# Kernel tuning notes

Hardware: AMD Instinct MI355X
Metric: run time of the kernel (lower is better)

Reference implementation:

```python
import jax, jax.numpy as jnp
import numpy as np

K_DIM = 128       # self.dim (PCA components)
SIGMA = 1.0       # cov = eye(dim) * sigma
NUM_LABELS = 10   # label vocabulary for private_label


def setup_inputs() -> dict:
    key = jax.random.key(0)
    k1, k2 = jax.random.split(key)
    mu = jax.random.normal(k1, (8192, 1024), dtype=jnp.float32)
    private_label = jax.random.randint(k2, (8192,), 0, NUM_LABELS, dtype=jnp.int32)
    return {"mu": mu, "private_label": private_label}


def _forward(mu, private_label):
    B = mu.shape[0]
    k = K_DIM
    x = mu.reshape(B, -1)
    # PCA: center, SVD of X^T, project onto top-k left singular vectors of X^T
    xc = x - jnp.mean(x, axis=0)
    U, _, _ = jnp.linalg.svd(xc.T, full_matrices=False)  # U: [D, min(D,B)]
    z = xc @ U[:, :k]                                    # [B, k]

    cov = jnp.eye(k, dtype=z.dtype) * SIGMA
    mu_total = jnp.mean(z, axis=0)                       # [k]
    diff = z - mu_total                                  # [B, k]
    Sigma_total = cov + (diff.T @ diff) / B              # [k, k]

    seg = private_label
    counts = jax.ops.segment_sum(jnp.ones((B,), z.dtype), seg, num_segments=NUM_LABELS)
    safe_c = jnp.where(counts > 0, counts, 1.0)
    sum_mu = jax.ops.segment_sum(z, seg, num_segments=NUM_LABELS)  # [L, k]
    mu_F = sum_mu / safe_c[:, None]                                # [L, k]

    # NOTE: faithful to source — per-label covariance uses diff w.r.t. mu_total
    onehot = jax.nn.one_hot(seg, NUM_LABELS, dtype=z.dtype)        # [B, L]
    masked = onehot[:, :, None] * diff[:, None, :]                 # [B, L, k]
    Sigma_sum = jnp.einsum('bli,bj->lij', masked, diff)            # [L, k, k]
    Sigma_F = cov + Sigma_sum / safe_c[:, None, None]              # [L, k, k]

    # KL( N(mu_F, Sigma_F) || N(mu_total, Sigma_total) ) per label
    Sinv = jnp.linalg.inv(Sigma_total)
    tr = jnp.einsum('ij,lji->l', Sinv, Sigma_F)
    d = mu_total[None, :] - mu_F                                   # [L, k]
    maha = jnp.einsum('li,ij,lj->l', d, Sinv, d)
    _, logdet_t = jnp.linalg.slogdet(Sigma_total)
    _, logdet_f = jnp.linalg.slogdet(Sigma_F)
    kl = 0.5 * (tr + maha - k + logdet_t - logdet_f)               # [L]

    present = counts > 0
    result = jnp.sum(jnp.where(present, kl, 0.0))
    n_keys = jnp.sum(present).astype(z.dtype)
    return result / (n_keys * B)


def reference(mu, private_label):
    return _forward(mu, private_label)
```

## Files before the change

### kernel.cpp

```cpp
#include <hip/hip_runtime.h>
#include <hip/hip_bf16.h>
#include <math.h>


#define B_N 8192
#define D_N 1024
#define K_N 128
#define M_N 256
#define NLAB 10

__device__ __forceinline__ float hashf(unsigned x) {
  x ^= x >> 16; x *= 0x7feb352du; x ^= x >> 15; x *= 0x846ca68bu; x ^= x >> 16;
  return (float)(x >> 8) * (1.0f / 16777216.0f) - 0.5f;
}

struct GArgs {
  const float* A; const float* B; float* C;
  int lda, ldb, ldc, K;
  float alpha;
  const float* C1; float b1; int ldc1;
  const float* C2; float b2; int ldc2;
  const float* r1u; const float* r1v; float r1c;
  const float* radd; float raddc;
  float addI;
  float* Cp; size_t mn; int pn;
  float* out2; float sc2, dg2;
};

template <bool AKM, bool BT>
__global__ __launch_bounds__(256)
void gemm_k(GArgs g) {
  __shared__ __align__(16) float AsRaw[2304];
  __shared__ __align__(16) float Bs[2176];
  const int tid = threadIdx.x;
  const int tx = tid & 15, ty = tid >> 4;
  const int i0 = blockIdx.x * 64, j0 = blockIdx.y * 64;
  const int ks = gridDim.z;
  const int Kc = g.K / ks;
  const int kbeg = blockIdx.z * Kc, kend = kbeg + Kc;
  float acc[4][4] = {};
  for (int k0 = kbeg; k0 < kend; k0 += 32) {
    if (AKM) {
#pragma unroll
      for (int p = 0; p < 2; ++p) {
        int f4 = tid + p * 256;
        int kk = f4 >> 4, i4 = f4 & 15;
        *(float4*)(AsRaw + kk * 68 + i4 * 4) =
            *(const float4*)(g.A + (size_t)(k0 + kk) * g.lda + i0 + i4 * 4);
      }
    } else {
#pragma unroll
      for (int p = 0; p < 2; ++p) {
        int f4 = tid + p * 256;
        int ii = f4 >> 3, k4 = f4 & 7;
        *(float4*)(AsRaw + ii * 36 + k4 * 4) =
            *(const float4*)(g.A + (size_t)(i0 + ii) * g.lda + k0 + k4 * 4);
      }
    }
    if (BT) {
#pragma unroll
      for (int p = 0; p < 8; ++p) {
        int idx = tid + p * 256;
        int jj = idx >> 5, kk = idx & 31;
        Bs[kk * 68 + jj] = g.B[(size_t)(j0 + jj) * g.ldb + k0 + kk];
      }
    } else {
#pragma unroll
      for (int p = 0; p < 2; ++p) {
        int f4 = tid + p * 256;
        int kk = f4 >> 4, j4 = f4 & 15;
        *(float4*)(Bs + kk * 68 + j4 * 4) =
            *(const float4*)(g.B + (size_t)(k0 + kk) * g.ldb + j0 + j4 * 4);
      }
    }
    __syncthreads();
#pragma unroll 8
    for (int kk = 0; kk < 32; ++kk) {
      float ra[4], rb[4];
      if (AKM) {
        const float4 va = *(const float4*)(AsRaw + kk * 68 + ty * 4);
        ra[0] = va.x; ra[1] = va.y; ra[2] = va.z; ra[3] = va.w;
      } else {
#pragma unroll
        for (int r = 0; r < 4; ++r) ra[r] = AsRaw[(ty * 4 + r) * 36 + kk];
      }
      const float4 vb = *(const float4*)(Bs + kk * 68 + tx * 4);
      rb[0] = vb.x; rb[1] = vb.y; rb[2] = vb.z; rb[3] = vb.w;
#pragma unroll
      for (int r = 0; r < 4; ++r)
#pragma unroll
        for (int c = 0; c < 4; ++c) acc[r][c] += ra[r] * rb[c];
    }
    __syncthreads();
  }
  if (ks > 1) {
    float* dst = g.Cp + (size_t)blockIdx.z * g.mn;
#pragma unroll
    for (int r = 0; r < 4; ++r)
#pragma unroll
      for (int c = 0; c < 4; ++c) {
        int gi = i0 + ty * 4 + r, gj = j0 + tx * 4 + c;
        dst[(size_t)gi * g.pn + gj] = g.alpha * acc[r][c];
      }
  } else {
#pragma unroll
    for (int r = 0; r < 4; ++r)
#pragma unroll
      for (int c = 0; c < 4; ++c) {
        int gi = i0 + ty * 4 + r, gj = j0 + tx * 4 + c;
        float v = g.alpha * acc[r][c];
        if (g.C1) v += g.b1 * g.C1[(size_t)gi * g.ldc1 + gj];
        if (g.C2) v += g.b2 * g.C2[(size_t)gi * g.ldc2 + gj];
        if (g.r1u) v += g.r1c * g.r1u[gi] * g.r1v[gj];
        if (g.radd) v += g.raddc * g.radd[gj];
        if (g.addI != 0.0f && gi == gj) v += g.addI;
        g.C[(size_t)gi * g.ldc + gj] = v;
      }
  }
}

struct CArgs {
  const float* P; float* C; size_t mn; int N, ldc, ks;
  const float* C1; float b1; int ldc1;
  const float* C2; float b2; int ldc2;
  const float* r1u; const float* r1v; float r1c;
  const float* radd; float raddc;
  float addI;
  float* out2; float sc2, dg2;
};

__global__ __launch_bounds__(256)
void combine_k(CArgs c) {
  size_t idx = (size_t)blockIdx.x * 256 + threadIdx.x;
  if (idx >= c.mn) return;
  int i = (int)(idx / c.N), j = (int)(idx % c.N);
  float s = 0.0f;
  for (int z = 0; z < c.ks; ++z) s += c.P[(size_t)z * c.mn + idx];
  if (c.C1) s += c.b1 * c.C1[(size_t)i * c.ldc1 + j];
  if (c.C2) s += c.b2 * c.C2[(size_t)i * c.ldc2 + j];
  if (c.r1u) s += c.r1c * c.r1u[i] * c.r1v[j];
  if (c.radd) s += c.raddc * c.radd[j];
  if (c.addI != 0.0f && i == j) s += c.addI;
  c.C[(size_t)i * c.ldc + j] = s;
  if (c.out2) c.out2[(size_t)i * c.N + j] = s * c.sc2 + ((i == j) ? c.dg2 : 0.0f);
}

__global__ __launch_bounds__(256)
void scaleshift_k(const float* in, float* out, int n, float sc, float dg) {
  size_t idx = (size_t)blockIdx.x * 256 + threadIdx.x;
  if (idx >= (size_t)n * n) return;
  int i = (int)(idx / n), j = (int)(idx % n);
  out[idx] = in[idx] * sc + ((i == j) ? dg : 0.0f);
}

__global__ __launch_bounds__(256)
void symscale_k(const float* in, float* out, int n, float sc, float dg) {
  size_t idx = (size_t)blockIdx.x * 256 + threadIdx.x;
  if (idx >= (size_t)n * n) return;
  int i = (int)(idx / n), j = (int)(idx % n);
  out[idx] = 0.5f * (in[idx] + in[(size_t)j * n + i]) * sc + ((i == j) ? dg : 0.0f);
}

__global__ __launch_bounds__(256)
void colmean_part_k(const float* x, double* part) {
  int col = blockIdx.x * 256 + threadIdx.x;
  int rs = blockIdx.y;
  double acc = 0.0;
  for (int r = rs * 512; r < (rs + 1) * 512; ++r)
    acc += (double)x[(size_t)r * D_N + col];
  part[(size_t)rs * D_N + col] = acc;
}

__global__ __launch_bounds__(256)
void colmean_comb_k(const double* part, float* m) {
  int col = blockIdx.x * 256 + threadIdx.x;
  double acc = 0.0;
  for (int rs = 0; rs < 16; ++rs) acc += part[(size_t)rs * D_N + col];
  m[col] = (float)(acc / (double)B_N);
}

__global__ void inits_k(float* S, int n, unsigned seed) {
  int i = blockIdx.x * 256 + threadIdx.x;
  if (i < n) S[i] = hashf((unsigned)i * 2654435761u + seed);
}

__global__ __launch_bounds__(512)
void chol128_k(const float* Gin, int ldg, float* LinvT, double* logdet, float* Sinv) {
  __shared__ float A[128][132];
  __shared__ float Bm[128][132];
  __shared__ float Y[64][66];
  __shared__ float Dsh[128];
  __shared__ float sqv[128];
  const int tid = threadIdx.x;
  for (int idx = tid; idx < 128 * 128; idx += 512)
    A[idx >> 7][idx & 127] = Gin[(size_t)(idx >> 7) * ldg + (idx & 127)];
  for (int idx = tid; idx < 128 * 132; idx += 512)
    (&Bm[0][0])[idx] = 0.0f;
  __syncthreads();
  for (int b = 0; b < 8; ++b) {
    const int o = b * 16;
    if (tid < 64) {
      const int lane = tid;
      float ra[16], rb[16], Dv[16];
#pragma unroll
      for (int q = 0; q < 16; ++q) {
        ra[q] = A[lane][o + q];
        rb[q] = A[lane + 64][o + q];
      }
#pragma unroll
      for (int jj = 0; jj < 16; ++jj) {
        const int c = o + jj;
        float pj = (c < 64) ? __shfl(ra[jj], c) : __shfl(rb[jj], c - 64);
        pj = fmaxf(pj, 1e-30f);
        Dv[jj] = pj;
        const float rdj = 1.0f / pj;
        const float ua = ra[jj] * rdj;
        const float ub = rb[jj] * rdj;
#pragma unroll
        for (int t = jj + 1; t < 16; ++t) {
          const int rt = o + t;
          float atj = (rt < 64) ? __shfl(ra[jj], rt) : __shfl(rb[jj], rt - 64);
          ra[t] -= ua * atj;
          rb[t] -= ub * atj;
        }
        ra[jj] = ua; rb[jj] = ub;
      }
#pragma unroll
      for (int q = 0; q < 16; ++q) {
        A[lane][o + q] = ra[q];
        A[lane + 64][o + q] = rb[q];
      }
      if (lane < 16) Dsh[o + lane] = Dv[lane];
    }
    __syncthreads();
    if (o + 16 < 128) {
      const int tx = tid & 15, ty = tid >> 4;
      for (int i = o + 16 + ty; i < 128; i += 32) {
        float w[16];
#pragma unroll
        for (int q = 0; q < 16; ++q) w[q] = A[i][o + q] * Dsh[o + q];
        for (int t = o + 16 + tx; t <= i; t += 16) {
          float s = A[i][t];
#pragma unroll
          for (int q = 0; q < 16; ++q) s -= w[q] * A[t][o + q];
          A[i][t] = s;
        }
      }
    }
    __syncthreads();
  }
  if (logdet && tid == 0) {
    double s = 0.0;
    for (int j = 0; j < 128; ++j) s += log((double)Dsh[j]);
    *logdet = s;
  }
  if (tid < 128) sqv[tid] = sqrtf(Dsh[tid]);
  __syncthreads();
  for (int idx = tid; idx < 128 * 128; idx += 512) {
    int i = idx >> 7, j = idx & 127;
    if (j <= i) A[i][j] *= sqv[j];
  }
  __syncthreads();
  if (tid < 128) {
    const int ob = (tid >> 6) * 64;
    const int c = tid & 63;
    for (int i = c; i < 64; ++i) {
      float s = (i == c) ? 1.0f : 0.0f;
      for (int t = c; t < i; ++t) s -= A[ob + i][ob + t] * Bm[ob + c][ob + t];
      Bm[ob + c][ob + i] = s / A[ob + i][ob + i];
    }
  }
  __syncthreads();
  for (int idx = tid; idx < 64 * 64; idx += 512) {
    int t = idx >> 6, c = idx & 63;
    float s = 0.0f;
    for (int s2 = c; s2 < 64; ++s2) s += A[64 + t][s2] * Bm[c][s2];
    Y[t][c] = s;
  }
  __syncthreads();
  for (int idx = tid; idx < 64 * 64; idx += 512) {
    int a = idx >> 6, c = idx & 63;
    float s = 0.0f;
    for (int t = 0; t <= a; ++t) s -= Bm[64 + t][64 + a] * Y[t][c];
    Bm[c][64 + a] = s;
  }
  __syncthreads();
  if (LinvT)
    for (int idx = tid; idx < 128 * 128; idx += 512)
      LinvT[idx] = Bm[idx >> 7][idx & 127];
  if (Sinv)
    for (int idx = tid; idx < 128 * 128; idx += 512) {
      int i = idx >> 7, j = idx & 127;
      int t0 = (i > j) ? i : j;
      float s = 0.0f;
      for (int t = t0; t < 128; ++t) s += Bm[i][t] * Bm[j][t];
      Sinv[idx] = s;
    }
}

__global__ __launch_bounds__(128)
void mw_k(const float* m, const float* W, float* mW) {
  int j = threadIdx.x;
  double acc = 0.0;
  for (int c = 0; c < D_N; ++c) acc += (double)m[c] * (double)W[(size_t)c * K_N + j];
  mW[j] = (float)acc;
}

__global__ __launch_bounds__(256)
void count_sort_k(const int* lab, int* perm, int* counts, int* offs) {
  __shared__ int cnt[NLAB][256];
  __shared__ int labOff[NLAB + 1];
  const int tid = threadIdx.x;
  int lc[NLAB];
#pragma unroll
  for (int l = 0; l < NLAB; ++l) lc[l] = 0;
  for (int r = tid * 32; r < tid * 32 + 32; ++r) {
    int l = lab[r]; l = (l < 0) ? 0 : (l > 9 ? 9 : l);
    lc[l]++;
  }
#pragma unroll
  for (int l = 0; l < NLAB; ++l) cnt[l][tid] = lc[l];
  __syncthreads();
  if (tid < NLAB) {
    int run = 0;
    for (int i = 0; i < 256; ++i) { int v = cnt[tid][i]; cnt[tid][i] = run; run += v; }
    counts[tid] = run;
  }
  __syncthreads();
  if (tid == 0) {
    int run = 0;
    for (int l = 0; l < NLAB; ++l) { labOff[l] = run; run += counts[l]; }
    labOff[NLAB] = run;
    for (int l = 0; l <= NLAB; ++l) offs[l] = labOff[l];
  }
  __syncthreads();
  int lc2[NLAB];
#pragma unroll
  for (int l = 0; l < NLAB; ++l) lc2[l] = 0;
  for (int r = tid * 32; r < tid * 32 + 32; ++r) {
    int l = lab[r]; l = (l < 0) ? 0 : (l > 9 ? 9 : l);
    int pos = labOff[l] + cnt[l][tid] + lc2[l];
    lc2[l]++;
    perm[pos] = r;
  }
}

__global__ __launch_bounds__(256)
void gather_k(const float* z, const int* perm, float* zs) {
  int g = blockIdx.x * 256 + threadIdx.x;
  int row = g >> 5, q = g & 31;
  const float4* zf = (const float4*)z;
  float4* of = (float4*)zs;
  of[(size_t)row * 32 + q] = zf[(size_t)perm[row] * 32 + q];
}

__global__ __launch_bounds__(128)
void labstat_part_k(const float* zs, const int* offs, double* part) {
  int l = blockIdx.x >> 3, s = blockIdx.x & 7;
  int j = threadIdx.x;
  int r0, r1;
  if (l < NLAB) {
    int st = offs[l], en = offs[l + 1], len = en - st;
    r0 = st + (int)(((long long)len * s) >> 3);
    r1 = st + (int)(((long long)len * (s + 1)) >> 3);
  } else {
    r0 = s * 1024; r1 = r0 + 1024;
  }
  double acc = 0.0;
  for (int r = r0; r < r1; ++r) acc += (double)zs[(size_t)r * K_N + j];
  part[((size_t)l * 8 + s) * K_N + j] = acc;
}

__global__ __launch_bounds__(128)
void labstat_comb_k(const double* part, float* sum_mu, float* muT) {
  int j = threadIdx.x;
  for (int l = 0; l < NLAB; ++l) {
    double a = 0.0;
    for (int s = 0; s < 8; ++s) a += part[((size_t)l * 8 + s) * K_N + j];
    sum_mu[l * K_N + j] = (float)a;
  }
  double t = 0.0;
  for (int s = 0; s < 8; ++s) t += part[((size_t)NLAB * 8 + s) * K_N + j];
  muT[j] = (float)(t / (double)B_N);
}

__global__ __launch_bounds__(256)
void sigsum_k(const float* zs, const int* offs, const float* muT, float* SigS) {
  int l = blockIdx.x >> 2, t = blockIdx.x & 3;
  int i0 = (t >> 1) * 64, j0 = (t & 1) * 64;
  __shared__ float Zi[32][66], Zj[32][66];
  __shared__ float muL[128];
  int tid = threadIdx.x, tx = tid & 15, ty = tid >> 4;
  if (tid < 128) muL[tid] = muT[tid];
  __syncthreads();
  int start = offs[l], end = offs[l + 1];
  float acc[4][4] = {};
  for (int base = start; base < end; base += 32) {
#pragma unroll
    for (int p = 0; p < 8; ++p) {
      int idx = tid + p * 256;
      int rr = idx >> 6, cc = idx & 63;
      int r = base + rr;
      float vi = 0.0f, vj = 0.0f;
      if (r < end) {
        vi = zs[(size_t)r * K_N + i0 + cc] - muL[i0 + cc];
        vj = zs[(size_t)r * K_N + j0 + cc] - muL[j0 + cc];
      }
      Zi[rr][cc] = vi; Zj[rr][cc] = vj;
    }
    __syncthreads();
    for (int rr = 0; rr < 32; ++rr) {
      float ra[4], rb[4];
#pragma unroll
      for (int r = 0; r < 4; ++r) ra[r] = Zi[rr][ty * 4 + r];
#pragma unroll
      for (int c = 0; c < 4; ++c) rb[c] = Zj[rr][tx * 4 + c];
#pragma unroll
      for (int r = 0; r < 4; ++r)
#pragma unroll
        for (int c = 0; c < 4; ++c) acc[r][c] += ra[r] * rb[c];
    }
    __syncthreads();
  }
#pragma unroll
  for (int r = 0; r < 4; ++r)
#pragma unroll
    for (int c = 0; c < 4; ++c)
      SigS[((size_t)l * K_N + i0 + ty * 4 + r) * K_N + j0 + tx * 4 + c] = acc[r][c];
}

__global__ __launch_bounds__(256)
void sigt_comb_k(const float* SigS, float* SigT) {
  int idx = blockIdx.x * 256 + threadIdx.x;
  int i = idx >> 7, j = idx & 127;
  double s = 0.0;
  for (int l = 0; l < NLAB; ++l) s += (double)SigS[(size_t)l * 16384 + idx];
  SigT[idx] = (float)(s / (double)B_N) + ((i == j) ? 1.0f : 0.0f);
}

__global__ __launch_bounds__(512)
void perlabel_k(const float* SigS, const float* Sinv, const float* mu,
                const float* sum_mu, const int* counts, const double* logdet_t,
                double* klout, int* present) {
  int l = blockIdx.x, tid = threadIdx.x;
  __shared__ float Amat[128][132];
  __shared__ double red[512];
  __shared__ float dv[128];
  __shared__ float Dsh[128];
  int cnt = counts[l];
  float sc = (cnt > 0) ? (float)cnt : 1.0f;
  for (int idx = tid; idx < 128 * 128; idx += 512) {
    int i = idx >> 7, j = idx & 127;
    Amat[i][j] = SigS[((size_t)l * K_N + i) * K_N + j] / sc + ((i == j) ? 1.0f : 0.0f);
  }
  if (tid < 128) dv[tid] = mu[tid] - sum_mu[l * K_N + tid] / sc;
  __syncthreads();
  double tr = 0.0, mh = 0.0;
  for (int idx = tid; idx < 128 * 128; idx += 512) {
    int i = idx >> 7, j = idx & 127;
    double sv = (double)Sinv[idx];
    tr += sv * (double)Amat[i][j];
    mh += sv * (double)dv[i] * (double)dv[j];
  }
  red[tid] = tr; __syncthreads();
  for (int off = 256; off > 0; off >>= 1) { if (tid < off) red[tid] += red[tid + off]; __syncthreads(); }
  double trv = red[0]; __syncthreads();
  red[tid] = mh; __syncthreads();
  for (int off = 256; off > 0; off >>= 1) { if (tid < off) red[tid] += red[tid + off]; __syncthreads(); }
  double mhv = red[0]; __syncthreads();
  for (int b = 0; b < 8; ++b) {
    const int o = b * 16;
    if (tid < 64) {
      const int lane = tid;
      float ra[16], rb[16], Dv[16];
#pragma unroll
      for (int q = 0; q < 16; ++q) {
        ra[q] = Amat[lane][o + q];
        rb[q] = Amat[lane + 64][o + q];
      }
#pragma unroll
      for (int jj = 0; jj < 16; ++jj) {
        const int c = o + jj;
        float pj = (c < 64) ? __shfl(ra[jj], c) : __shfl(rb[jj], c - 64);
        pj = fmaxf(pj, 1e-30f);
        Dv[jj] = pj;
        const float rdj = 1.0f / pj;
        const float ua = ra[jj] * rdj;
        const float ub = rb[jj] * rdj;
#pragma unroll
        for (int t = jj + 1; t < 16; ++t) {
          const int rt = o + t;
          float atj = (rt < 64) ? __shfl(ra[jj], rt) : __shfl(rb[jj], rt - 64);
          ra[t] -= ua * atj;
          rb[t] -= ub * atj;
        }
        ra[jj] = ua; rb[jj] = ub;
      }
#pragma unroll
      for (int q = 0; q < 16; ++q) {
        Amat[lane][o + q] = ra[q];
        Amat[lane + 64][o + q] = rb[q];
      }
      if (lane < 16) Dsh[o + lane] = Dv[lane];
    }
    __syncthreads();
    if (o + 16 < 128) {
      const int tx = tid & 15, ty = tid >> 4;
      for (int i = o + 16 + ty; i < 128; i += 32) {
        float w[16];
#pragma unroll
        for (int q = 0; q < 16; ++q) w[q] = Amat[i][o + q] * Dsh[o + q];
        for (int t = o + 16 + tx; t <= i; t += 16) {
          float s = Amat[i][t];
#pragma unroll
          for (int q = 0; q < 16; ++q) s -= w[q] * Amat[t][o + q];
          Amat[i][t] = s;
        }
      }
    }
    __syncthreads();
  }
  if (tid == 0) {
    double ld = 0.0;
    for (int j = 0; j < 128; ++j) ld += log((double)Dsh[j]);
    klout[l] = 0.5 * (trv + mhv - 128.0 + logdet_t[0] - ld);
    present[l] = (cnt > 0) ? 1 : 0;
  }
}

__global__ void finalize_k(const double* kl, const int* present, float* out) {
  if (threadIdx.x == 0 && blockIdx.x == 0) {
    double s = 0.0; int np = 0;
    for (int l = 0; l < NLAB; ++l)
      if (present[l]) { s += kl[l]; np++; }
    out[0] = (float)((np > 0) ? s / ((double)np * (double)B_N) : 0.0);
  }
}

static inline GArgs mkg(const float* A, int lda, const float* B, int ldb,
                        float* C, int ldc, int K, float alpha) {
  GArgs g{};
  g.A = A; g.B = B; g.C = C; g.lda = lda; g.ldb = ldb; g.ldc = ldc;
  g.K = K; g.alpha = alpha;
  return g;
}

static inline void run_g(hipStream_t st, bool akm, bool bt, GArgs g,
                         int M, int N, int ks, float* Ppart) {
  if (ks > 1) {
    g.Cp = Ppart; g.mn = (size_t)M * N; g.pn = N;
    dim3 grid(M / 64, N / 64, ks);
    if (akm)     hipLaunchKernelGGL((gemm_k<true, false>),  grid, dim3(256), 0, st, g);
    else if (bt) hipLaunchKernelGGL((gemm_k<false, true>),  grid, dim3(256), 0, st, g);
    else         hipLaunchKernelGGL((gemm_k<false, false>), grid, dim3(256), 0, st, g);
    CArgs c{Ppart, g.C, (size_t)M * N, N, g.ldc, ks,
            g.C1, g.b1, g.ldc1, g.C2, g.b2, g.ldc2,
            g.r1u, g.r1v, g.r1c, g.radd, g.raddc, g.addI,
            g.out2, g.sc2, g.dg2};
    hipLaunchKernelGGL(combine_k, dim3((unsigned)(((size_t)M * N + 255) / 256)),
                       dim3(256), 0, st, c);
  } else {
    dim3 grid(M / 64, N / 64);
    if (akm)     hipLaunchKernelGGL((gemm_k<true, false>),  grid, dim3(256), 0, st, g);
    else if (bt) hipLaunchKernelGGL((gemm_k<false, true>),  grid, dim3(256), 0, st, g);
    else         hipLaunchKernelGGL((gemm_k<false, false>), grid, dim3(256), 0, st, g);
  }
}

extern "C" void kernel_launch(void* const* d_in, const int* in_sizes, int n_in,
                              void* d_out, int out_size, void* d_ws, size_t ws_size,
                              hipStream_t stream) {
  const float* x = (const float*)d_in[0];
  const int* lab = (const int*)d_in[1];
  float* out = (float*)d_out;

  size_t off = 0;
  auto alloc = [&](size_t nbytes) -> void* {
    void* r = (void*)((char*)d_ws + off);
    off += ((nbytes + 255) / 256) * 256;
    return r;
  };
  float*  m     = (float*) alloc(D_N * 4);
  float*  Cn    = (float*) alloc((size_t)D_N * D_N * 4);
  float*  At    = (float*) alloc((size_t)D_N * D_N * 4);
  float*  T2    = (float*) alloc((size_t)D_N * D_N * 4);
  float*  Fo    = (float*) alloc((size_t)D_N * D_N * 4);
  float*  SA    = (float*) alloc((size_t)D_N * M_N * 4);
  float*  SB    = (float*) alloc((size_t)D_N * M_N * 4);
  float*  SC    = (float*) alloc((size_t)D_N * M_N * 4);
  float*  G256  = (float*) alloc((size_t)M_N * M_N * 4);
  float*  Tm    = (float*) alloc((size_t)M_N * M_N * 4);
  float*  Li11T = (float*) alloc((size_t)K_N * K_N * 4);
  float*  Li22T = (float*) alloc((size_t)K_N * K_N * 4);
  float*  L21b  = (float*) alloc((size_t)K_N * K_N * 4);
  float*  S22b  = (float*) alloc((size_t)K_N * K_N * 4);
  float*  Pb    = (float*) alloc((size_t)K_N * K_N * 4);
  float*  XTb   = (float*) alloc((size_t)K_N * K_N * 4);
  float*  Tt    = (float*) alloc((size_t)M_N * M_N * 4);
  float*  T2i   = (float*) alloc((size_t)M_N * M_N * 4);
  float*  T4i   = (float*) alloc((size_t)M_N * M_N * 4);
  float*  F6i   = (float*) alloc((size_t)M_N * M_N * 4);
  float*  VA    = (float*) alloc((size_t)M_N * K_N * 4);
  float*  VB    = (float*) alloc((size_t)M_N * K_N * 4);
  float*  G128  = (float*) alloc((size_t)K_N * K_N * 4);
  float*  Li128 = (float*) alloc((size_t)K_N * K_N * 4);
  float*  Wa    = (float*) alloc((size_t)D_N * K_N * 4);
  float*  Wb    = (float*) alloc((size_t)D_N * K_N * 4);
  float*  mW    = (float*) alloc(K_N * 4);
  double* partM = (double*)alloc((size_t)16 * D_N * 8);
  double* partL = (double*)alloc((size_t)11 * 8 * K_N * 8);
  float*  sumMu = (float*) alloc(NLAB * K_N * 4);
  float*  muT   = (float*) alloc(K_N * 4);
  float*  SigT  = (float*) alloc((size_t)K_N * K_N * 4);
  float*  Sinv  = (float*) alloc((size_t)K_N * K_N * 4);
  float*  SigS  = (float*) alloc((size_t)NLAB * K_N * K_N * 4);
  double* logdet_t = (double*)alloc(16);
  double* klv      = (double*)alloc(NLAB * 8);
  int*    counts = (int*)alloc(16 * 4);
  int*    offs   = (int*)alloc(16 * 4);
  int*    present= (int*)alloc(16 * 4);
  int*    perm   = (int*)alloc(B_N * 4);
  float*  T4   = At;
  float*  F12i = G256;
  float*  zs   = At;
  float*  z    = T2;
  size_t rem = (ws_size > off) ? (ws_size - off) : 0;
  int KS = 1;
  if (rem >= (size_t)16 * 1024 * 1024 + 4096) KS = 4;
  else if (rem >= (size_t)8 * 1024 * 1024 + 4096) KS = 2;
  float* Ppart = (float*)alloc((size_t)KS * 4 * 1024 * 1024);
  const int gks = (KS == 4) ? 8 : KS;
  (void)in_sizes; (void)n_in; (void)out_size;

  hipLaunchKernelGGL(colmean_part_k, dim3(4, 16), dim3(256), 0, stream, x, partM);
  hipLaunchKernelGGL(colmean_comb_k, dim3(4), dim3(256), 0, stream, partM, m);
  {
    GArgs g = mkg(x, D_N, x, D_N, Cn, D_N, B_N, 1.0f / (float)B_N);
    g.r1u = m; g.r1v = m; g.r1c = -1.0f;
    if (KS > 1) { g.out2 = At; g.sc2 = 1.6f; g.dg2 = -1.0f; }
    run_g(stream, true, false, g, D_N, D_N, KS, Ppart);
    if (KS == 1)
      hipLaunchKernelGGL(scaleshift_k, dim3((D_N * D_N + 255) / 256), dim3(256),
                         0, stream, Cn, At, D_N, 1.6f, -1.0f);
  }

  {
    GArgs g = mkg(At, D_N, At, D_N, T2, D_N, D_N, 2.0f);
    g.addI = -1.0f;
    run_g(stream, true, false, g, D_N, D_N, KS, Ppart);
    g = mkg(T2, D_N, T2, D_N, T4, D_N, D_N, 2.0f);
    g.addI = -1.0f;
    run_g(stream, true, false, g, D_N, D_N, KS, Ppart);
    g = mkg(T2, D_N, T4, D_N, Fo, D_N, D_N, 2.0f);
    g.C1 = T2; g.b1 = -1.0f; g.ldc1 = D_N;
    run_g(stream, true, false, g, D_N, D_N, KS, Ppart);
  }

  auto qr256 = [&](float* S, float* Snew) {
    GArgs g = mkg(S, M_N, S, M_N, G256, M_N, D_N, 1.0f);
    run_g(stream, true, false, g, M_N, M_N, gks, Ppart);
    hipLaunchKernelGGL(chol128_k, dim3(1), dim3(512), 0, stream,
                       G256, M_N, Li11T, (double*)nullptr, (float*)nullptr);
    g = mkg(G256 + 128 * M_N, M_N, Li11T, K_N, L21b, K_N, K_N, 1.0f);
    run_g(stream, false, false, g, K_N, K_N, 1, nullptr);
    g = mkg(L21b, K_N, L21b, K_N, S22b, K_N, K_N, -1.0f);
    g.C1 = G256 + 128 * M_N + 128; g.b1 = 1.0f; g.ldc1 = M_N;
    run_g(stream, false, true, g, K_N, K_N, 1, nullptr);
    hipLaunchKernelGGL(chol128_k, dim3(1), dim3(512), 0, stream,
                       S22b, K_N, Li22T, (double*)nullptr, (float*)nullptr);
    g = mkg(L21b, K_N, Li11T, K_N, Pb, K_N, K_N, 1.0f);
    run_g(stream, false, true, g, K_N, K_N, 1, nullptr);
    g = mkg(Pb, K_N, Li22T, K_N, XTb, K_N, K_N, -1.0f);
    run_g(stream, true, false, g, K_N, K_N, 1, nullptr);
    g = mkg(S, M_N, Li11T, K_N, Snew, M_N, K_N, 1.0f);
    run_g(stream, false, false, g, D_N, K_N, 1, nullptr);
    g = mkg(S, M_N, XTb, K_N, Snew + 128, M_N, K_N, 1.0f);
    run_g(stream, false, false, g, D_N, K_N, 1, nullptr);
    g = mkg(S + 128, M_N, Li22T, K_N, Snew + 128, M_N, K_N, 1.0f);
    g.C1 = Snew + 128; g.b1 = 1.0f; g.ldc1 = M_N;
    run_g(stream, false, false, g, D_N, K_N, 1, nullptr);
  };

  hipLaunchKernelGGL(inits_k, dim3((D_N * M_N + 255) / 256), dim3(256), 0, stream,
                     SA, D_N * M_N, 12345u);
  float* Scur = SA; float* t1 = SB; float* t2 = SC;
  for (int seg = 0; seg < 2; ++seg) {
    GArgs g = mkg(Fo, D_N, Scur, M_N, t1, M_N, D_N, 1.0f);
    run_g(stream, true, false, g, D_N, M_N, KS, Ppart);
    qr256(t1, t2);
    float* t = Scur; Scur = t2; t2 = t;
  }

  {
    GArgs g = mkg(Cn, D_N, Scur, M_N, t1, M_N, D_N, 1.0f);
    run_g(stream, true, false, g, D_N, M_N, KS, Ppart);
    g = mkg(Scur, M_N, t1, M_N, Tm, M_N, D_N, 1.0f);
    run_g(stream, true, false, g, M_N, M_N, gks, Ppart);
  }

  hipLaunchKernelGGL(symscale_k, dim3((M_N * M_N + 255) / 256), dim3(256), 0,
                     stream, Tm, Tt, M_N, 1.0f / 0.635f, -1.0f);
  {
    GArgs g = mkg(Tt, M_N, Tt, M_N, T2i, M_N, M_N, 2.0f);
    g.addI = -1.0f;
    run_g(stream, true, false, g, M_N, M_N, 1, nullptr);
    g = mkg(T2i, M_N, T2i, M_N, T4i, M_N, M_N, 2.0f);
    g.addI = -1.0f;
    run_g(stream, true, false, g, M_N, M_N, 1, nullptr);
    g = mkg(T2i, M_N, T4i, M_N, F6i, M_N, M_N, 2.0f);
    g.C1 = T2i; g.b1 = -1.0f; g.ldc1 = M_N;
    run_g(stream, true, false, g, M_N, M_N, 1, nullptr);
    g = mkg(F6i, M_N, F6i, M_N, F12i, M_N, M_N, 2.0f);
    g.addI = -1.0f;
    run_g(stream, true, false, g, M_N, M_N, 1, nullptr);
  }

  hipLaunchKernelGGL(inits_k, dim3((M_N * K_N + 255) / 256), dim3(256), 0, stream,
                     VA, M_N * K_N, 777u);
  {
    GArgs g = mkg(F12i, M_N, VA, K_N, VB, K_N, M_N, 1.0f);
    run_g(stream, true, false, g, M_N, K_N, 1, nullptr);
    g = mkg(VB, K_N, VB, K_N, G128, K_N, M_N, 1.0f);
    run_g(stream, true, false, g, K_N, K_N, 1, nullptr);
    hipLaunchKernelGGL(chol128_k, dim3(1), dim3(512), 0, stream,
                       G128, K_N, Li128, (double*)nullptr, (float*)nullptr);
    g = mkg(VB, K_N, Li128, K_N, VA, K_N, K_N, 1.0f);
    run_g(stream, false, false, g, M_N, K_N, 1, nullptr);
  }

  {
    GArgs g = mkg(Scur, M_N, VA, K_N, Wa, K_N, M_N, 1.0f);
    run_g(stream, false, false, g, D_N, K_N, 1, nullptr);
    g = mkg(Wa, K_N, Wa, K_N, G128, K_N, D_N, 1.0f);
    run_g(stream, true, false, g, K_N, K_N, gks, Ppart);
    hipLaunchKernelGGL(chol128_k, dim3(1), dim3(512), 0, stream,
                       G128, K_N, Li128, (double*)nullptr, (float*)nullptr);
    g = mkg(Wa, K_N, Li128, K_N, Wb, K_N, K_N, 1.0f);
    run_g(stream, false, false, g, D_N, K_N, 1, nullptr);
  }

  hipLaunchKernelGGL(mw_k, dim3(1), dim3(128), 0, stream, m, Wb, mW);
  {
    GArgs g = mkg(x, D_N, Wb, K_N, z, K_N, D_N, 1.0f);
    g.radd = mW; g.raddc = -1.0f;
    run_g(stream, false, false, g, B_N, K_N, KS, Ppart);
  }

  hipLaunchKernelGGL(count_sort_k, dim3(1), dim3(256), 0, stream,
                     lab, perm, counts, offs);
  hipLaunchKernelGGL(gather_k, dim3(B_N * 32 / 256), dim3(256), 0, stream,
                     z, perm, zs);

  hipLaunchKernelGGL(labstat_part_k, dim3(11 * 8), dim3(128), 0, stream,
                     zs, offs, partL);
  hipLaunchKernelGGL(labstat_comb_k, dim3(1), dim3(128), 0, stream,
                     partL, sumMu, muT);

  hipLaunchKernelGGL(sigsum_k, dim3(NLAB * 4), dim3(256), 0, stream,
                     zs, offs, muT, SigS);
  hipLaunchKernelGGL(sigt_comb_k, dim3(64), dim3(256), 0, stream, SigS, SigT);
  hipLaunchKernelGGL(chol128_k, dim3(1), dim3(512), 0, stream,
                     SigT, K_N, (float*)nullptr, logdet_t, Sinv);

  hipLaunchKernelGGL(perlabel_k, dim3(NLAB), dim3(512), 0, stream,
                     SigS, Sinv, muT, sumMu, counts, logdet_t, klv, present);
  hipLaunchKernelGGL(finalize_k, dim3(1), dim3(64), 0, stream, klv, present, out);
}
```

Measured before the change: 2.500 ms.

## Fuse blocked Cholesky-QR into single kernel producing full R inverse

Replaces the multi-launch 256-wide Cholesky-QR (two chol128 launches plus six small GEMMs) with one qrf_k kernel. It computes both diagonal Cholesky inverses, the Schur complement and the off-diagonal block of R^-1 in shared memory, then applies the whole 256x256 R^-1 to S with one GEMM. It also changes shared-memory padding from 132 to 129, factors the LDL code into a shared helper, and adds a larger split-K option for the covariance GEMM. The fused kernel runs on a single workgroup and does 128^3-sized GEMMs on one CU, which may serialize work that the separate GEMM launches spread across the device.

```diff
diff --git a/kernel.cpp b/kernel.cpp
--- a/kernel.cpp
+++ b/kernel.cpp
@@ -184,19 +184,8 @@
   if (i < n) S[i] = hashf((unsigned)i * 2654435761u + seed);
 }
 
-__global__ __launch_bounds__(512)
-void chol128_k(const float* Gin, int ldg, float* LinvT, double* logdet, float* Sinv) {
-  __shared__ float A[128][132];
-  __shared__ float Bm[128][132];
-  __shared__ float Y[64][66];
-  __shared__ float Dsh[128];
-  __shared__ float sqv[128];
-  const int tid = threadIdx.x;
-  for (int idx = tid; idx < 128 * 128; idx += 512)
-    A[idx >> 7][idx & 127] = Gin[(size_t)(idx >> 7) * ldg + (idx & 127)];
-  for (int idx = tid; idx < 128 * 132; idx += 512)
-    (&Bm[0][0])[idx] = 0.0f;
-  __syncthreads();
+__device__ __forceinline__
+void ldl128(float (&A)[128][129], float* Dsh, int tid) {
   for (int b = 0; b < 8; ++b) {
     const int o = b * 16;
     if (tid < 64) {
@@ -230,7 +219,9 @@
         A[lane][o + q] = ra[q];
         A[lane + 64][o + q] = rb[q];
       }
-      if (lane < 16) Dsh[o + lane] = Dv[lane];
+#pragma unroll
+      for (int q = 0; q < 16; ++q)
+        if (lane == q) Dsh[o + q] = Dv[q];
     }
     __syncthreads();
     if (o + 16 < 128) {
@@ -249,11 +240,15 @@
     }
     __syncthreads();
   }
-  if (logdet && tid == 0) {
-    double s = 0.0;
-    for (int j = 0; j < 128; ++j) s += log((double)Dsh[j]);
-    *logdet = s;
-  }
+}
+
+__device__ __forceinline__
+void cholinv128(float (&A)[128][129], float (&Bm)[128][129],
+                float (&Y)[64][65], float* Dsh, float* sqv, int tid) {
+  for (int idx = tid; idx < 128 * 129; idx += 512)
+    (&Bm[0][0])[idx] = 0.0f;
+  __syncthreads();
+  ldl128(A, Dsh, tid);
   if (tid < 128) sqv[tid] = sqrtf(Dsh[tid]);
   __syncthreads();
   for (int idx = tid; idx < 128 * 128; idx += 512) {
@@ -285,6 +280,24 @@
     Bm[c][64 + a] = s;
   }
   __syncthreads();
+}
+
+__global__ __launch_bounds__(512)
+void chol128_k(const float* Gin, int ldg, float* LinvT, double* logdet, float* Sinv) {
+  __shared__ float A[128][129];
+  __shared__ float Bm[128][129];
+  __shared__ float Y[64][65];
+  __shared__ float Dsh[128], sqv[128];
+  const int tid = threadIdx.x;
+  for (int idx = tid; idx < 128 * 128; idx += 512)
+    A[idx >> 7][idx & 127] = Gin[(size_t)(idx >> 7) * ldg + (idx & 127)];
+  __syncthreads();
+  cholinv128(A, Bm, Y, Dsh, sqv, tid);
+  if (logdet && tid == 0) {
+    double s = 0.0;
+    for (int j = 0; j < 128; ++j) s += log((double)Dsh[j]);
+    *logdet = s;
+  }
   if (LinvT)
     for (int idx = tid; idx < 128 * 128; idx += 512)
       LinvT[idx] = Bm[idx >> 7][idx & 127];
@@ -296,6 +309,128 @@
       for (int t = t0; t < 128; ++t) s += Bm[i][t] * Bm[j][t];
       Sinv[idx] = s;
     }
+}
+
+__global__ __launch_bounds__(512)
+void qrf_k(const float* G, int ldg, float* Rinv, float* Pg) {
+  __shared__ float A[128][129];
+  __shared__ float Bm[128][129];
+  __shared__ float Y[64][65];
+  __shared__ float Dsh[128], sqv[128];
+  const int tid = threadIdx.x;
+  const int jl = tid & 31;
+  const int il = tid >> 5;
+  for (int idx = tid; idx < 128 * 128; idx += 512)
+    A[idx >> 7][idx & 127] = G[(size_t)(idx >> 7) * ldg + (idx & 127)];
+  __syncthreads();
+  cholinv128(A, Bm, Y, Dsh, sqv, tid);
+  for (int idx = tid; idx < 128 * 128; idx += 512) {
+    int k = idx >> 7, j = idx & 127;
+    Rinv[(size_t)k * 256 + j] = Bm[k][j];
+    Rinv[(size_t)(128 + k) * 256 + j] = 0.0f;
+  }
+  __syncthreads();
+  {
+    float acc[8][4] = {};
+    for (int t = 0; t < 128; ++t) {
+      float bv[4];
+#pragma unroll
+      for (int c = 0; c < 4; ++c) bv[c] = Bm[t][jl + 32 * c];
+#pragma unroll
+      for (int r = 0; r < 8; ++r) {
+        float gv = G[(size_t)(128 + il + 16 * r) * ldg + t];
+#pragma unroll
+        for (int c = 0; c < 4; ++c) acc[r][c] += gv * bv[c];
+      }
+    }
+    __syncthreads();
+#pragma unroll
+    for (int r = 0; r < 8; ++r)
+#pragma unroll
+      for (int c = 0; c < 4; ++c) {
+        int i = il + 16 * r, j = jl + 32 * c;
+        A[i][j] = acc[r][c];
+        Pg[(size_t)i * 128 + j] = acc[r][c];
+      }
+  }
+  __syncthreads();
+  {
+    float acc[8][4] = {};
+    for (int t = 0; t < 128; ++t) {
+      float bv[4];
+#pragma unroll
+      for (int c = 0; c < 4; ++c) bv[c] = A[jl + 32 * c][t];
+#pragma unroll
+      for (int r = 0; r < 8; ++r) {
+        float av = A[il + 16 * r][t];
+#pragma unroll
+        for (int c = 0; c < 4; ++c) acc[r][c] += av * bv[c];
+      }
+    }
+    __syncthreads();
+#pragma unroll
+    for (int r = 0; r < 8; ++r)
+#pragma unroll
+      for (int c = 0; c < 4; ++c) {
+        int i = il + 16 * r, j = jl + 32 * c;
+        Bm[i][j] = G[(size_t)(128 + i) * ldg + 128 + j] - acc[r][c];
+      }
+  }
+  __syncthreads();
+  for (int idx = tid; idx < 128 * 128; idx += 512) {
+    int i = idx >> 7, j = idx & 127;
+    float v = Bm[i][j];
+    __syncthreads();
+    A[i][j] = v;
+    __syncthreads();
+  }
+  __syncthreads();
+  cholinv128(A, Bm, Y, Dsh, sqv, tid);
+  for (int idx = tid; idx < 128 * 128; idx += 512) {
+    int k = idx >> 7, j = idx & 127;
+    Rinv[(size_t)(128 + k) * 256 + 128 + j] = Bm[k][j];
+  }
+  __syncthreads();
+  {
+    float acc[8][4] = {};
+    for (int s = 0; s < 128; ++s) {
+      float bv[4];
+#pragma unroll
+      for (int c = 0; c < 4; ++c) bv[c] = Bm[s][jl + 32 * c];
+#pragma unroll
+      for (int r = 0; r < 8; ++r) {
+        float pv = Pg[(size_t)s * 128 + il + 16 * r];
+#pragma unroll
+        for (int c = 0; c < 4; ++c) acc[r][c] += pv * bv[c];
+      }
+    }
+    __syncthreads();
+#pragma unroll
+    for (int r = 0; r < 8; ++r)
+#pragma unroll
+      for (int c = 0; c < 4; ++c)
+        A[il + 16 * r][jl + 32 * c] = acc[r][c];
+  }
+  __syncthreads();
+  {
+    float acc[8][4] = {};
+    for (int t = 0; t < 128; ++t) {
+      float bv[4];
+#pragma unroll
+      for (int c = 0; c < 4; ++c) bv[c] = A[t][jl + 32 * c];
+#pragma unroll
+      for (int r = 0; r < 8; ++r) {
+        float rv = Rinv[(size_t)(il + 16 * r) * 256 + t];
+#pragma unroll
+        for (int c = 0; c < 4; ++c) acc[r][c] += rv * bv[c];
+      }
+    }
+#pragma unroll
+    for (int r = 0; r < 8; ++r)
+#pragma unroll
+      for (int c = 0; c < 4; ++c)
+        Rinv[(size_t)(il + 16 * r) * 256 + 128 + jl + 32 * c] = -acc[r][c];
+  }
 }
 
 __global__ __launch_bounds__(128)
@@ -443,7 +578,7 @@
                 const float* sum_mu, const int* counts, const double* logdet_t,
                 double* klout, int* present) {
   int l = blockIdx.x, tid = threadIdx.x;
-  __shared__ float Amat[128][132];
+  __shared__ float Amat[128][129];
   __shared__ double red[512];
   __shared__ float dv[128];
   __shared__ float Dsh[128];
@@ -468,58 +603,7 @@
   red[tid] = mh; __syncthreads();
   for (int off = 256; off > 0; off >>= 1) { if (tid < off) red[tid] += red[tid + off]; __syncthreads(); }
   double mhv = red[0]; __syncthreads();
-  for (int b = 0; b < 8; ++b) {
-    const int o = b * 16;
-    if (tid < 64) {
-      const int lane = tid;
-      float ra[16], rb[16], Dv[16];
-#pragma unroll
-      for (int q = 0; q < 16; ++q) {
-        ra[q] = Amat[lane][o + q];
-        rb[q] = Amat[lane + 64][o + q];
-      }
-#pragma unroll
-      for (int jj = 0; jj < 16; ++jj) {
-        const int c = o + jj;
-        float pj = (c < 64) ? __shfl(ra[jj], c) : __shfl(rb[jj], c - 64);
-        pj = fmaxf(pj, 1e-30f);
-        Dv[jj] = pj;
-        const float rdj = 1.0f / pj;
-        const float ua = ra[jj] * rdj;
-        const float ub = rb[jj] * rdj;
-#pragma unroll
-        for (int t = jj + 1; t < 16; ++t) {
-          const int rt = o + t;
-          float atj = (rt < 64) ? __shfl(ra[jj], rt) : __shfl(rb[jj], rt - 64);
-          ra[t] -= ua * atj;
-          rb[t] -= ub * atj;
-        }
-        ra[jj] = ua; rb[jj] = ub;
-      }
-#pragma unroll
-      for (int q = 0; q < 16; ++q) {
-        Amat[lane][o + q] = ra[q];
-        Amat[lane + 64][o + q] = rb[q];
-      }
-      if (lane < 16) Dsh[o + lane] = Dv[lane];
-    }
-    __syncthreads();
-    if (o + 16 < 128) {
-      const int tx = tid & 15, ty = tid >> 4;
-      for (int i = o + 16 + ty; i < 128; i += 32) {
-        float w[16];
-#pragma unroll
-        for (int q = 0; q < 16; ++q) w[q] = Amat[i][o + q] * Dsh[o + q];
-        for (int t = o + 16 + tx; t <= i; t += 16) {
-          float s = Amat[i][t];
-#pragma unroll
-          for (int q = 0; q < 16; ++q) s -= w[q] * Amat[t][o + q];
-          Amat[i][t] = s;
-        }
-      }
-    }
-    __syncthreads();
-  }
+  ldl128(Amat, Dsh, tid);
   if (tid == 0) {
     double ld = 0.0;
     for (int j = 0; j < 128; ++j) ld += log((double)Dsh[j]);
@@ -590,12 +674,8 @@
   float*  SC    = (float*) alloc((size_t)D_N * M_N * 4);
   float*  G256  = (float*) alloc((size_t)M_N * M_N * 4);
   float*  Tm    = (float*) alloc((size_t)M_N * M_N * 4);
-  float*  Li11T = (float*) alloc((size_t)K_N * K_N * 4);
-  float*  Li22T = (float*) alloc((size_t)K_N * K_N * 4);
-  float*  L21b  = (float*) alloc((size_t)K_N * K_N * 4);
-  float*  S22b  = (float*) alloc((size_t)K_N * K_N * 4);
-  float*  Pb    = (float*) alloc((size_t)K_N * K_N * 4);
-  float*  XTb   = (float*) alloc((size_t)K_N * K_N * 4);
+  float*  Rb    = (float*) alloc((size_t)M_N * M_N * 4);
+  float*  Pg2   = (float*) alloc((size_t)K_N * K_N * 4);
   float*  Tt    = (float*) alloc((size_t)M_N * M_N * 4);
   float*  T2i   = (float*) alloc((size_t)M_N * M_N * 4);
   float*  T4i   = (float*) alloc((size_t)M_N * M_N * 4);
@@ -625,11 +705,13 @@
   float*  zs   = At;
   float*  z    = T2;
   size_t rem = (ws_size > off) ? (ws_size - off) : 0;
-  int KS = 1;
-  if (rem >= (size_t)16 * 1024 * 1024 + 4096) KS = 4;
-  else if (rem >= (size_t)8 * 1024 * 1024 + 4096) KS = 2;
-  float* Ppart = (float*)alloc((size_t)KS * 4 * 1024 * 1024);
-  const int gks = (KS == 4) ? 8 : KS;
+  int KS = 1, KSC = 1;
+  size_t pbytes = 0;
+  if (rem >= (size_t)33 * 1024 * 1024)      { KSC = 8; KS = 4; pbytes = (size_t)32 * 1024 * 1024; }
+  else if (rem >= (size_t)17 * 1024 * 1024) { KSC = 4; KS = 4; pbytes = (size_t)16 * 1024 * 1024; }
+  else if (rem >= (size_t)9 * 1024 * 1024)  { KSC = 2; KS = 2; pbytes = (size_t)8 * 1024 * 1024; }
+  float* Ppart = pbytes ? (float*)alloc(pbytes) : nullptr;
+  const int gks = (KS >= 4) ? 8 : KS;
   (void)in_sizes; (void)n_in; (void)out_size;
 
   hipLaunchKernelGGL(colmean_part_k, dim3(4, 16), dim3(256), 0, stream, x, partM);
@@ -637,9 +719,9 @@
   {
     GArgs g = mkg(x, D_N, x, D_N, Cn, D_N, B_N, 1.0f / (float)B_N);
     g.r1u = m; g.r1v = m; g.r1c = -1.0f;
-    if (KS > 1) { g.out2 = At; g.sc2 = 1.6f; g.dg2 = -1.0f; }
-    run_g(stream, true, false, g, D_N, D_N, KS, Ppart);
-    if (KS == 1)
+    if (KSC > 1) { g.out2 = At; g.sc2 = 1.6f; g.dg2 = -1.0f; }
+    run_g(stream, true, false, g, D_N, D_N, KSC, Ppart);
+    if (KSC == 1)
       hipLaunchKernelGGL(scaleshift_k, dim3((D_N * D_N + 255) / 256), dim3(256),
                          0, stream, Cn, At, D_N, 1.6f, -1.0f);
   }
@@ -659,26 +741,9 @@
   auto qr256 = [&](float* S, float* Snew) {
     GArgs g = mkg(S, M_N, S, M_N, G256, M_N, D_N, 1.0f);
     run_g(stream, true, false, g, M_N, M_N, gks, Ppart);
-    hipLaunchKernelGGL(chol128_k, dim3(1), dim3(512), 0, stream,
-                       G256, M_N, Li11T, (double*)nullptr, (float*)nullptr);
-    g = mkg(G256 + 128 * M_N, M_N, Li11T, K_N, L21b, K_N, K_N, 1.0f);
-    run_g(stream, false, false, g, K_N, K_N, 1, nullptr);
-    g = mkg(L21b, K_N, L21b, K_N, S22b, K_N, K_N, -1.0f);
-    g.C1 = G256 + 128 * M_N + 128; g.b1 = 1.0f; g.ldc1 = M_N;
-    run_g(stream, false, true, g, K_N, K_N, 1, nullptr);
-    hipLaunchKernelGGL(chol128_k, dim3(1), dim3(512), 0, stream,
-                       S22b, K_N, Li22T, (double*)nullptr, (float*)nullptr);
-    g = mkg(L21b, K_N, Li11T, K_N, Pb, K_N, K_N, 1.0f);
-    run_g(stream, false, true, g, K_N, K_N, 1, nullptr);
-    g = mkg(Pb, K_N, Li22T, K_N, XTb, K_N, K_N, -1.0f);
-    run_g(stream, true, false, g, K_N, K_N, 1, nullptr);
-    g = mkg(S, M_N, Li11T, K_N, Snew, M_N, K_N, 1.0f);
-    run_g(stream, false, false, g, D_N, K_N, 1, nullptr);
-    g = mkg(S, M_N, XTb, K_N, Snew + 128, M_N, K_N, 1.0f);
-    run_g(stream, false, false, g, D_N, K_N, 1, nullptr);
-    g = mkg(S + 128, M_N, Li22T, K_N, Snew + 128, M_N, K_N, 1.0f);
-    g.C1 = Snew + 128; g.b1 = 1.0f; g.ldc1 = M_N;
-    run_g(stream, false, false, g, D_N, K_N, 1, nullptr);
+    hipLaunchKernelGGL(qrf_k, dim3(1), dim3(512), 0, stream, G256, M_N, Rb, Pg2);
+    g = mkg(S, M_N, Rb, M_N, Snew, M_N, M_N, 1.0f);
+    run_g(stream, false, false, g, D_N, M_N, KS, Ppart);
   };
 
   hipLaunchKernelGGL(inits_k, dim3((D_N * M_N + 255) / 256), dim3(256), 0, stream,
```

Result: no change. 2.534 ms (+1.4%).
